# Optimization experiments

Hardware: AMD Instinct MI355X
Metric: run time of the kernel (lower is better)

Reference implementation:

```python
import jax, jax.numpy as jnp
import numpy as np

N, NFEAT, NHID, NCLASS, NHEAD = 8192, 512, 64, 16, 4
ALPHA = 0.1  # leaky relu slope
NEG = -9e15


def setup_inputs() -> dict:
    key = jax.random.key(0)
    ks = jax.random.split(key, 7)
    x = jax.random.normal(ks[0], (N, NFEAT), dtype=jnp.float32)
    adj = (jax.random.uniform(ks[1], (N, N)) < 0.05).astype(jnp.float32)
    # per-head params: W [H, nfeat, nhid], a [H, 2*nhid] (xavier-ish scale)
    W = jax.random.normal(ks[2], (NHEAD, NFEAT, NHID), dtype=jnp.float32) * (1.0 / np.sqrt(NFEAT))
    a = jax.random.normal(ks[3], (NHEAD, 2 * NHID), dtype=jnp.float32) * (1.0 / np.sqrt(NHID))
    W_out = jax.random.normal(ks[4], (NHEAD * NHID, NCLASS), dtype=jnp.float32) * (1.0 / np.sqrt(NHEAD * NHID))
    a_out = jax.random.normal(ks[5], (2 * NCLASS,), dtype=jnp.float32) * (1.0 / np.sqrt(NCLASS))
    return {"x": x, "adj": adj, "W": W, "a": a, "W_out": W_out, "a_out": a_out}


def _gat_layer(h, adj, Wk, ak):
    """Dense pyGAT GraphAttentionLayer (eval mode, dropout = identity)."""
    d = Wk.shape[1]
    Wh = h @ Wk                         # [N, d]
    f1 = Wh @ ak[:d]                    # [N]
    f2 = Wh @ ak[d:]                    # [N]
    e = jax.nn.leaky_relu(f1[:, None] + f2[None, :], negative_slope=ALPHA)  # [N, N]
    att = jax.nn.softmax(jnp.where(adj > 0, e, NEG), axis=1)
    return att @ Wh                     # [N, d]


def reference(x, adj, W, a, W_out, a_out):
    # eval mode: F.dropout is identity
    heads = jax.vmap(lambda Wk, ak: jax.nn.elu(_gat_layer(x, adj, Wk, ak)))(W, a)  # [H, N, nhid]
    h = jnp.transpose(heads, (1, 0, 2)).reshape(x.shape[0], -1)                    # [N, H*nhid]
    out = jax.nn.elu(_gat_layer(h, adj, W_out, a_out))                             # [N, nclass]
    return jax.nn.log_softmax(out, axis=1)
```

## Files before the change

kernel.cpp:

```cpp
#include <hip/hip_runtime.h>
#include <hip/hip_bf16.h>

#define NN 8192
#define NFEAT 512
#define NHID 64
#define NCLASS 16
#define NHEAD 4
#define ALPHA 0.1f
#define CAP 768
#define ZSPLIT 4
#define JPB (NN / ZSPLIT)
#define DCH 128

typedef short bf16x8 __attribute__((ext_vector_type(8)));
typedef float f32x4 __attribute__((ext_vector_type(4)));
typedef float fv4 __attribute__((ext_vector_type(4)));

__device__ __forceinline__ float lrelu(float x) { return fmaxf(x, ALPHA * x); }
__device__ __forceinline__ float elu(float x) { return x > 0.f ? x : __expf(x) - 1.f; }
__device__ __forceinline__ short f2b(float x) {
  union { __bf16 b; short s; } c; c.b = (__bf16)x; return c.s;
}
__device__ __forceinline__ float b2f(short x) {
  union { unsigned int u; float f; } c; c.u = ((unsigned int)(unsigned short)x) << 16; return c.f;
}

#define UPF(w, v, A0, A1)                                  \
  {                                                        \
    const float lo_ = __uint_as_float((v) << 16);          \
    const float hi_ = __uint_as_float((v) & 0xffff0000u);  \
    (A0) += (w) * lo_;                                     \
    (A1) += (w) * hi_;                                     \
  }

__global__ __launch_bounds__(256) void k_wprep(const float* __restrict__ W,
                                               short* __restrict__ WB) {
  __shared__ float t[64][65];
  const int h = blockIdx.y;
  const int k0 = blockIdx.x * 64;
  const int tid = threadIdx.x;
#pragma unroll
  for (int it = 0; it < 16; ++it) {
    const int r = it * 4 + (tid >> 6), c = tid & 63;
    t[r][c] = W[((size_t)h * NFEAT + k0 + r) * NHID + c];
  }
  __syncthreads();
#pragma unroll
  for (int it = 0; it < 16; ++it) {
    const int d = it * 4 + (tid >> 6), k = tid & 63;
    WB[((size_t)h * NHID + d) * NFEAT + k0 + k] = f2b(t[k][d]);
  }
}

__global__ __launch_bounds__(256) void k_prep1(const float* __restrict__ x,
                                               const short* __restrict__ WB,
                                               const float* __restrict__ a,
                                               short* __restrict__ Whf,
                                               float* __restrict__ f1i,
                                               float* __restrict__ f2i) {
  __shared__ short tile[64][72];
  const int bid = blockIdx.x;
  const int h = bid >> 7;
  const int bm = (bid & 127) * 64;
  const int tid = threadIdx.x;
  const int wv = tid >> 6, lane = tid & 63;
  const int mr = lane & 15, kg = lane >> 4;
  f32x4 acc0 = {0.f, 0.f, 0.f, 0.f}, acc1 = acc0, acc2 = acc0, acc3 = acc0;
  const float* ap = x + (size_t)(bm + wv * 16 + mr) * NFEAT + kg * 8;
  const short* bp = WB + ((size_t)h * NHID + mr) * NFEAT + kg * 8;
#pragma unroll 2
  for (int k0 = 0; k0 < NFEAT; k0 += 32) {
    const float4 xa = *reinterpret_cast<const float4*>(ap);
    const float4 xb = *reinterpret_cast<const float4*>(ap + 4);
    bf16x8 af;
    af[0] = f2b(xa.x); af[1] = f2b(xa.y); af[2] = f2b(xa.z); af[3] = f2b(xa.w);
    af[4] = f2b(xb.x); af[5] = f2b(xb.y); af[6] = f2b(xb.z); af[7] = f2b(xb.w);
    const bf16x8 b0 = *reinterpret_cast<const bf16x8*>(bp);
    const bf16x8 b1 = *reinterpret_cast<const bf16x8*>(bp + 16 * NFEAT);
    const bf16x8 b2 = *reinterpret_cast<const bf16x8*>(bp + 32 * NFEAT);
    const bf16x8 b3 = *reinterpret_cast<const bf16x8*>(bp + 48 * NFEAT);
    acc0 = __builtin_amdgcn_mfma_f32_16x16x32_bf16(af, b0, acc0, 0, 0, 0);
    acc1 = __builtin_amdgcn_mfma_f32_16x16x32_bf16(af, b1, acc1, 0, 0, 0);
    acc2 = __builtin_amdgcn_mfma_f32_16x16x32_bf16(af, b2, acc2, 0, 0, 0);
    acc3 = __builtin_amdgcn_mfma_f32_16x16x32_bf16(af, b3, acc3, 0, 0, 0);
    ap += 32; bp += 32;
  }
  float a1v[4], a2v[4];
#pragma unroll
  for (int c = 0; c < 4; ++c) {
    a1v[c] = a[h * 128 + mr + c * 16];
    a2v[c] = a[h * 128 + 64 + mr + c * 16];
  }
#pragma unroll
  for (int q = 0; q < 4; ++q) {
    float s1 = acc0[q] * a1v[0] + acc1[q] * a1v[1] + acc2[q] * a1v[2] + acc3[q] * a1v[3];
    float s2 = acc0[q] * a2v[0] + acc1[q] * a2v[1] + acc2[q] * a2v[2] + acc3[q] * a2v[3];
#pragma unroll
    for (int off = 1; off < 16; off <<= 1) {
      s1 += __shfl_xor(s1, off);
      s2 += __shfl_xor(s2, off);
    }
    if (mr == 0) {
      const int i = bm + wv * 16 + kg * 4 + q;
      f1i[(size_t)i * 4 + h] = s1;
      f2i[(size_t)i * 4 + h] = s2;
    }
  }
#pragma unroll
  for (int q = 0; q < 4; ++q) {
    const int r = wv * 16 + kg * 4 + q;
    tile[r][mr +  0] = f2b(acc0[q]);
    tile[r][mr + 16] = f2b(acc1[q]);
    tile[r][mr + 32] = f2b(acc2[q]);
    tile[r][mr + 48] = f2b(acc3[q]);
  }
  __syncthreads();
#pragma unroll
  for (int it = 0; it < 2; ++it) {
    const int jbl = (tid >> 6) + it * 4;
    const int d = tid & 63;
    bf16x8 o;
#pragma unroll
    for (int jo = 0; jo < 8; ++jo) o[jo] = tile[jbl * 8 + jo][d];
    *reinterpret_cast<bf16x8*>(Whf +
        (((size_t)h * 1024 + (bm >> 3) + jbl) * 64 + d) * 8) = o;
  }
}

__global__ __launch_bounds__(256) void k_rmax(const float* __restrict__ src,
                                              float* __restrict__ dst, int n, int stride,
                                              int boff) {
  const float* p = src + (size_t)blockIdx.x * boff;
  float m = -1e30f;
  for (int k = threadIdx.x; k < n; k += 256) m = fmaxf(m, p[(size_t)k * stride]);
#pragma unroll
  for (int off = 32; off; off >>= 1) m = fmaxf(m, __shfl_xor(m, off));
  __shared__ float sm[4];
  if ((threadIdx.x & 63) == 0) sm[threadIdx.x >> 6] = m;
  __syncthreads();
  if (threadIdx.x == 0) dst[blockIdx.x] = fmaxf(fmaxf(sm[0], sm[1]), fmaxf(sm[2], sm[3]));
}

__global__ __launch_bounds__(256) void k_acbd(const float* __restrict__ f1i,
                                              const float* __restrict__ f2i,
                                              const float* __restrict__ f2max,
                                              float2* __restrict__ ACh,
                                              unsigned int* __restrict__ BDh) {
  const int idx = blockIdx.x * 256 + threadIdx.x;
  const int i = idx & (NN - 1);
  const int h = idx >> 13;
  const float fm = f2max[h];
  const float f1 = f1i[(size_t)i * 4 + h];
  const float f2 = f2i[(size_t)i * 4 + h];
  const float s = f1 + fm;
  const float mrow = fmaxf(s, 0.1f * s);
  float2 ac;
  ac.x = __expf(s - mrow);
  ac.y = __expf(0.1f * s - mrow);
  ACh[(size_t)h * NN + i] = ac;
  const float t = f2 - fm;
  const unsigned int B = (unsigned short)f2b(__expf(t));
  const unsigned int D = (unsigned short)f2b(__expf(0.1f * t));
  BDh[(size_t)h * NN + i] = B | (D << 16);
}

__global__ __launch_bounds__(256) void k_scan(const float* __restrict__ adj,
                                              unsigned int* __restrict__ bmask) {
  const fv4* a4 = reinterpret_cast<const fv4*>(adj);
  const int t0 = blockIdx.x * 256 + threadIdx.x;
#pragma unroll 4
  for (int it = 0; it < 32; ++it) {
    const int g = it * 524288 + t0;
    const fv4 v = __builtin_nontemporal_load(a4 + g);
    unsigned int nv = (unsigned int)((v.x > 0.f) | ((v.y > 0.f) << 1) |
                                     ((v.z > 0.f) << 2) | ((v.w > 0.f) << 3))
                      << ((threadIdx.x & 7) * 4);
    nv |= __shfl_xor(nv, 1);
    nv |= __shfl_xor(nv, 2);
    nv |= __shfl_xor(nv, 4);
    if ((threadIdx.x & 7) == 0) bmask[g >> 3] = nv;
  }
}

__global__ __launch_bounds__(256) void k_dense1z(const unsigned int* __restrict__ bmask,
                                                 const short* __restrict__ Whf,
                                                 const float2* __restrict__ ACh,
                                                 const unsigned int* __restrict__ BDh,
                                                 float* __restrict__ OpP,
                                                 float* __restrict__ rsP) {
  __shared__ short sm_b[16 * 64 * 8];
  __shared__ unsigned int sm_bd[DCH];
  __shared__ unsigned int sm_mask[64][5];
  const int i0 = blockIdx.x * 64;
  const int h = blockIdx.y;
  const int z = blockIdx.z;
  const int jb0 = z * JPB;
  const int tid = threadIdx.x;
  const int wv = tid >> 6, lane = tid & 63;
  const int mr = lane & 15, kg = lane >> 4;
  const int row_local = wv * 16 + mr;
  const float2 ac = ACh[(size_t)h * NN + i0 + row_local];
  f32x4 acc0 = {0.f, 0.f, 0.f, 0.f}, acc1 = acc0, acc2 = acc0, acc3 = acc0;
  float rs = 0.f;

  for (int jc = jb0; jc < jb0 + JPB; jc += DCH) {
    __syncthreads();
    {
      sm_mask[tid >> 2][tid & 3] =
          bmask[(size_t)(i0 + (tid >> 2)) * 256 + (jc >> 5) + (tid & 3)];
      if (tid < DCH) sm_bd[tid] = BDh[(size_t)h * NN + jc + tid];
      const uint4* src = reinterpret_cast<const uint4*>(
          Whf + ((size_t)h * 1024 + (jc >> 3)) * 512);
      uint4* dst = reinterpret_cast<uint4*>(sm_b);
#pragma unroll
      for (int u = 0; u < 4; ++u) dst[tid + u * 256] = src[tid + u * 256];
    }
    __syncthreads();
#pragma unroll
    for (int ks = 0; ks < DCH / 32; ++ks) {
      const int jl = ks * 32 + kg * 8;
      const uint4 bda = *reinterpret_cast<const uint4*>(&sm_bd[jl]);
      const uint4 bdb = *reinterpret_cast<const uint4*>(&sm_bd[jl + 4]);
      const unsigned int mb = (sm_mask[row_local][ks] >> (kg * 8)) & 0xffu;
      bf16x8 af;
#define MKW(e, bdw)                                              \
      {                                                          \
        const float Bf = __uint_as_float((bdw) << 16);           \
        const float Df = __uint_as_float((bdw) & 0xffff0000u);   \
        float w_ = fmaxf(ac.x * Bf, ac.y * Df);                  \
        w_ = ((mb >> (e)) & 1u) ? w_ : 0.f;                      \
        rs += w_;                                                \
        af[e] = f2b(w_);                                         \
      }
      MKW(0, bda.x) MKW(1, bda.y) MKW(2, bda.z) MKW(3, bda.w)
      MKW(4, bdb.x) MKW(5, bdb.y) MKW(6, bdb.z) MKW(7, bdb.w)
#undef MKW
      const short* wp = sm_b + ((size_t)(jl >> 3) * 64 + mr) * 8;
      const bf16x8 bf0 = *reinterpret_cast<const bf16x8*>(wp);
      const bf16x8 bf1 = *reinterpret_cast<const bf16x8*>(wp + 128);
      const bf16x8 bf2 = *reinterpret_cast<const bf16x8*>(wp + 256);
      const bf16x8 bf3 = *reinterpret_cast<const bf16x8*>(wp + 384);
      acc0 = __builtin_amdgcn_mfma_f32_16x16x32_bf16(af, bf0, acc0, 0, 0, 0);
      acc1 = __builtin_amdgcn_mfma_f32_16x16x32_bf16(af, bf1, acc1, 0, 0, 0);
      acc2 = __builtin_amdgcn_mfma_f32_16x16x32_bf16(af, bf2, acc2, 0, 0, 0);
      acc3 = __builtin_amdgcn_mfma_f32_16x16x32_bf16(af, bf3, acc3, 0, 0, 0);
    }
  }
  rs += __shfl_xor(rs, 16);
  rs += __shfl_xor(rs, 32);
  if (lane < 16)
    rsP[((size_t)z * NHEAD + h) * NN + i0 + wv * 16 + lane] = rs;
  float* op = OpP + (((size_t)z * NHEAD + h) * NN + i0) * 64;
#pragma unroll
  for (int q = 0; q < 4; ++q) {
    const int r = wv * 16 + kg * 4 + q;
    op[(size_t)r * 64 + mr +  0] = acc0[q];
    op[(size_t)r * 64 + mr + 16] = acc1[q];
    op[(size_t)r * 64 + mr + 32] = acc2[q];
    op[(size_t)r * 64 + mr + 48] = acc3[q];
  }
}

__global__ __launch_bounds__(256) void k_comb1(const float* __restrict__ OpP,
                                               const float* __restrict__ rsP,
                                               short* __restrict__ hcat) {
  const int idx = blockIdx.x * 256 + threadIdx.x;
  const int i = idx >> 8;
  const int hc = idx & 255;
  const int h = hc >> 6, d = hc & 63;
  float s = 0.f, rsum = 0.f;
#pragma unroll
  for (int z = 0; z < ZSPLIT; ++z) {
    s += OpP[(((size_t)z * NHEAD + h) * NN + i) * 64 + d];
    rsum += rsP[((size_t)z * NHEAD + h) * NN + i];
  }
  hcat[idx] = f2b(elu(s / rsum));
}

__global__ __launch_bounds__(256) void k_gemm2(const short* __restrict__ hcat,
                                               const float* __restrict__ Wout,
                                               const float* __restrict__ aout,
                                               short* __restrict__ Wh2B,
                                               float* __restrict__ f1o,
                                               float* __restrict__ f2o) {
  __shared__ float sW[NHEAD * NHID][NCLASS + 1];
  __shared__ float sh[16][NHEAD * NHID + 1];
  const int tid = threadIdx.x;
  const int r = tid >> 4, c = tid & 15;
  const int row = blockIdx.x * 16 + r;
  for (int u = tid; u < 256 * 16; u += 256) sW[u >> 4][u & 15] = Wout[u];
  for (int u = tid; u < 16 * 256; u += 256)
    sh[u >> 8][u & 255] = b2f(hcat[(size_t)(blockIdx.x * 16 + (u >> 8)) * 256 + (u & 255)]);
  __syncthreads();
  float acc = 0.f;
#pragma unroll 8
  for (int f = 0; f < 256; ++f) acc += sh[r][f] * sW[f][c];
  Wh2B[(size_t)row * NCLASS + c] = f2b(acc);
  float s1 = acc * aout[c];
  float s2 = acc * aout[NCLASS + c];
#pragma unroll
  for (int off = 8; off; off >>= 1) { s1 += __shfl_xor(s1, off); s2 += __shfl_xor(s2, off); }
  if (c == 0) { f1o[row] = s1; f2o[row] = s2; }
}

__global__ __launch_bounds__(256) void k_attn2(const unsigned int* __restrict__ bmask,
                                               const short* __restrict__ Wh2B,
                                               const float* __restrict__ f1o,
                                               const float* __restrict__ f2o,
                                               const float* __restrict__ f2omax,
                                               float* __restrict__ out) {
  __shared__ unsigned short idx[CAP];
  __shared__ unsigned int wj[CAP + 4];
  __shared__ float red[4][NCLASS];
  __shared__ float swp[4];
  __shared__ float sinvs;
  __shared__ int cnt;
  const int i = blockIdx.x;
  const int tid = threadIdx.x;
  const int wv = tid >> 6, lane = tid & 63;
  if (tid == 0) cnt = 0;
  __syncthreads();

  {
    unsigned int word = bmask[(size_t)i * 256 + tid];
    const int c = __popc(word);
    if (c) {
      int base = atomicAdd(&cnt, c);
      const int j0 = tid * 32;
      while (word) {
        const int b = __ffs(word) - 1;
        word &= word - 1;
        if (base < CAP) idx[base++] = (unsigned short)(j0 + b);
      }
    }
  }
  __syncthreads();
  const int n = min(cnt, CAP);
  if (tid < 4) wj[n + tid] = 0;

  const float f1r = f1o[i];
  const float mrow = lrelu(f1r + f2omax[0]);
  float sw = 0.f;
  for (int k = tid; k < n; k += 256) {
    const int j = idx[k];
    const float w = __expf(lrelu(f1r + f2o[j]) - mrow);
    wj[k] = ((unsigned int)(unsigned short)f2b(w) << 16) | (unsigned int)j;
    sw += w;
  }
#pragma unroll
  for (int off = 32; off; off >>= 1) sw += __shfl_xor(sw, off);
  if (lane == 0) swp[wv] = sw;
  __syncthreads();
  if (tid == 0) sinvs = 1.f / (swp[0] + swp[1] + swp[2] + swp[3]);
  __syncthreads();

  const int grp = tid >> 2, gl = tid & 3;
  float acc0 = 0.f, acc1 = 0.f, acc2 = 0.f, acc3 = 0.f;
  const short* wb = Wh2B + gl * 4;
  for (int kb = grp * 4; kb < n; kb += 256) {
    const uint4 pw = *reinterpret_cast<const uint4*>(wj + kb);
    const uint2 e0 = *reinterpret_cast<const uint2*>(wb + (size_t)(pw.x & 0xffffu) * NCLASS);
    const uint2 e1 = *reinterpret_cast<const uint2*>(wb + (size_t)(pw.y & 0xffffu) * NCLASS);
    const uint2 e2 = *reinterpret_cast<const uint2*>(wb + (size_t)(pw.z & 0xffffu) * NCLASS);
    const uint2 e3 = *reinterpret_cast<const uint2*>(wb + (size_t)(pw.w & 0xffffu) * NCLASS);
    const float w0 = __uint_as_float(pw.x & 0xffff0000u);
    const float w1 = __uint_as_float(pw.y & 0xffff0000u);
    const float w2 = __uint_as_float(pw.z & 0xffff0000u);
    const float w3 = __uint_as_float(pw.w & 0xffff0000u);
    UPF(w0, e0.x, acc0, acc1) UPF(w0, e0.y, acc2, acc3)
    UPF(w1, e1.x, acc0, acc1) UPF(w1, e1.y, acc2, acc3)
    UPF(w2, e2.x, acc0, acc1) UPF(w2, e2.y, acc2, acc3)
    UPF(w3, e3.x, acc0, acc1) UPF(w3, e3.y, acc2, acc3)
  }
  acc0 += __shfl_xor(acc0, 4);  acc1 += __shfl_xor(acc1, 4);
  acc2 += __shfl_xor(acc2, 4);  acc3 += __shfl_xor(acc3, 4);
  acc0 += __shfl_xor(acc0, 8);  acc1 += __shfl_xor(acc1, 8);
  acc2 += __shfl_xor(acc2, 8);  acc3 += __shfl_xor(acc3, 8);
  acc0 += __shfl_xor(acc0, 16); acc1 += __shfl_xor(acc1, 16);
  acc2 += __shfl_xor(acc2, 16); acc3 += __shfl_xor(acc3, 16);
  acc0 += __shfl_xor(acc0, 32); acc1 += __shfl_xor(acc1, 32);
  acc2 += __shfl_xor(acc2, 32); acc3 += __shfl_xor(acc3, 32);
  if (lane < 4) {
    red[wv][lane * 4 + 0] = acc0;
    red[wv][lane * 4 + 1] = acc1;
    red[wv][lane * 4 + 2] = acc2;
    red[wv][lane * 4 + 3] = acc3;
  }
  __syncthreads();
  if (tid < NCLASS) {
    const float s = red[0][tid] + red[1][tid] + red[2][tid] + red[3][tid];
    const float v = elu(s * sinvs);
    float vm = v;
#pragma unroll
    for (int off = 8; off; off >>= 1) vm = fmaxf(vm, __shfl_xor(vm, off, 16));
    float ex = __expf(v - vm);
#pragma unroll
    for (int off = 8; off; off >>= 1) ex += __shfl_xor(ex, off, 16);
    out[(size_t)i * NCLASS + tid] = v - vm - __logf(ex);
  }
}

extern "C" void kernel_launch(void* const* d_in, const int* in_sizes, int n_in,
                              void* d_out, int out_size, void* d_ws, size_t ws_size,
                              hipStream_t stream) {
  const float* x    = (const float*)d_in[0];
  const float* adj  = (const float*)d_in[1];
  const float* W    = (const float*)d_in[2];
  const float* a    = (const float*)d_in[3];
  const float* Wout = (const float*)d_in[4];
  const float* aout = (const float*)d_in[5];
  float* out = (float*)d_out;
  char* ws = (char*)d_ws;
  const size_t MB = 1048576;
  const size_t KB = 1024;

  unsigned int* bmask  = (unsigned int*)(ws);
  short* Whf           = (short*)(ws + 8 * MB);
  short* hcat          = (short*)(ws + 12 * MB);
  float* OpP           = (float*)(ws + 16 * MB);
  float* rsP           = (float*)(ws + 48 * MB);
  short* WB            = (short*)(ws + 49 * MB);
  float* f1i           = (float*)(ws + 49 * MB + 256 * KB);
  float* f2i           = (float*)(ws + 49 * MB + 384 * KB);
  float2* ACh          = (float2*)(ws + 49 * MB + 512 * KB);
  unsigned int* BDh    = (unsigned int*)(ws + 49 * MB + 768 * KB);
  float* f1o           = (float*)(ws + 49 * MB + 896 * KB);
  float* f2o           = (float*)(ws + 49 * MB + 928 * KB);
  short* Wh2B          = (short*)(ws + 49 * MB + 960 * KB);
  float* f2max         = (float*)(ws + 49 * MB + 1216 * KB);
  float* f2omax        = (float*)(ws + 49 * MB + 1216 * KB + 64);

  k_wprep<<<dim3(8, 4), 256, 0, stream>>>(W, WB);
  k_prep1<<<512, 256, 0, stream>>>(x, WB, a, Whf, f1i, f2i);
  k_rmax<<<NHEAD, 256, 0, stream>>>(f2i, f2max, NN, 4, 1);
  k_acbd<<<NN * NHEAD / 256, 256, 0, stream>>>(f1i, f2i, f2max, ACh, BDh);
  k_scan<<<2048, 256, 0, stream>>>(adj, bmask);
  k_dense1z<<<dim3(NN / 64, NHEAD, ZSPLIT), 256, 0, stream>>>(bmask, Whf, ACh, BDh, OpP, rsP);
  k_comb1<<<NN, 256, 0, stream>>>(OpP, rsP, hcat);
  k_gemm2<<<NN / 16, 256, 0, stream>>>(hcat, Wout, aout, Wh2B, f1o, f2o);
  k_rmax<<<1, 256, 0, stream>>>(f2o, f2omax, NN, 1, 0);
  k_attn2<<<NN, 256, 0, stream>>>(bmask, Wh2B, f1o, f2o, f2omax, out);
}
```

Before: 216.2 us.

## Replace sparse gather attention in layer 2 with dense MFMA split-K kernel

The second attention layer no longer compacts neighbor indices and gathers rows per node. It now uses a dense bitmask-driven MFMA kernel split into eight column chunks, with a new factored exp precompute (AC2/BD2), a tiled Wh2 layout written by gemm2, and a combine kernel that does ELU and log-softmax. This trades irregular gathers, atomics and a per-row workspace cap for regular dense tensor-core work over all 8192 columns, plus two extra launches and partial-sum traffic. A leftover dummy mask read was also added to dense1z.

```diff
diff --git a/kernel.cpp b/kernel.cpp
--- a/kernel.cpp
+++ b/kernel.cpp
@@ -7,10 +7,11 @@
 #define NCLASS 16
 #define NHEAD 4
 #define ALPHA 0.1f
-#define CAP 768
 #define ZSPLIT 4
 #define JPB (NN / ZSPLIT)
 #define DCH 128
+#define Z2 8
+#define JPB2 (NN / Z2)
 
 typedef short bf16x8 __attribute__((ext_vector_type(8)));
 typedef float f32x4 __attribute__((ext_vector_type(4)));
@@ -24,14 +25,6 @@
 __device__ __forceinline__ float b2f(short x) {
   union { unsigned int u; float f; } c; c.u = ((unsigned int)(unsigned short)x) << 16; return c.f;
 }
-
-#define UPF(w, v, A0, A1)                                  \
-  {                                                        \
-    const float lo_ = __uint_as_float((v) << 16);          \
-    const float hi_ = __uint_as_float((v) & 0xffff0000u);  \
-    (A0) += (w) * lo_;                                     \
-    (A1) += (w) * hi_;                                     \
-  }
 
 __global__ __launch_bounds__(256) void k_wprep(const float* __restrict__ W,
                                                short* __restrict__ WB) {
@@ -164,6 +157,27 @@
   BDh[(size_t)h * NN + i] = B | (D << 16);
 }
 
+__global__ __launch_bounds__(256) void k_acbd2(const float* __restrict__ f1o,
+                                               const float* __restrict__ f2o,
+                                               const float* __restrict__ f2omax,
+                                               float2* __restrict__ AC2,
+                                               unsigned int* __restrict__ BD2) {
+  const int i = blockIdx.x * 256 + threadIdx.x;
+  const float fm = f2omax[0];
+  const float f1 = f1o[i];
+  const float f2 = f2o[i];
+  const float s = f1 + fm;
+  const float mrow = fmaxf(s, 0.1f * s);
+  float2 ac;
+  ac.x = __expf(s - mrow);
+  ac.y = __expf(0.1f * s - mrow);
+  AC2[i] = ac;
+  const float t = f2 - fm;
+  const unsigned int B = (unsigned short)f2b(__expf(t));
+  const unsigned int D = (unsigned short)f2b(__expf(0.1f * t));
+  BD2[i] = B | (D << 16);
+}
+
 __global__ __launch_bounds__(256) void k_scan(const float* __restrict__ adj,
                                               unsigned int* __restrict__ bmask) {
   const fv4* a4 = reinterpret_cast<const fv4*>(adj);
@@ -221,14 +235,17 @@
       const int jl = ks * 32 + kg * 8;
       const uint4 bda = *reinterpret_cast<const uint4*>(&sm_bd[jl]);
       const uint4 bdb = *reinterpret_cast<const uint4*>(&sm_bd[jl + 4]);
-      const unsigned int mb = (sm_mask[row_local][ks] >> (kg * 8)) & 0xffu;
+      const unsigned int mb = (sm_mask[row_local][(jc - jb0) / 32 % 4 == 0 ? ks : ks]
+                               >> 0);
+      (void)mb;
+      const unsigned int mbb = (sm_mask[row_local][ks] >> (kg * 8)) & 0xffu;
       bf16x8 af;
 #define MKW(e, bdw)                                              \
       {                                                          \
         const float Bf = __uint_as_float((bdw) << 16);           \
         const float Df = __uint_as_float((bdw) & 0xffff0000u);   \
         float w_ = fmaxf(ac.x * Bf, ac.y * Df);                  \
-        w_ = ((mb >> (e)) & 1u) ? w_ : 0.f;                      \
+        w_ = ((mbb >> (e)) & 1u) ? w_ : 0.f;                     \
         rs += w_;                                                \
         af[e] = f2b(w_);                                         \
       }
@@ -280,7 +297,7 @@
 __global__ __launch_bounds__(256) void k_gemm2(const short* __restrict__ hcat,
                                                const float* __restrict__ Wout,
                                                const float* __restrict__ aout,
-                                               short* __restrict__ Wh2B,
+                                               short* __restrict__ Wh2f,
                                                float* __restrict__ f1o,
                                                float* __restrict__ f2o) {
   __shared__ float sW[NHEAD * NHID][NCLASS + 1];
@@ -295,7 +312,7 @@
   float acc = 0.f;
 #pragma unroll 8
   for (int f = 0; f < 256; ++f) acc += sh[r][f] * sW[f][c];
-  Wh2B[(size_t)row * NCLASS + c] = f2b(acc);
+  Wh2f[(((size_t)blockIdx.x * 2 + (r >> 3)) * 16 + c) * 8 + (r & 7)] = f2b(acc);
   float s1 = acc * aout[c];
   float s2 = acc * aout[NCLASS + c];
 #pragma unroll
@@ -303,101 +320,85 @@
   if (c == 0) { f1o[row] = s1; f2o[row] = s2; }
 }
 
-__global__ __launch_bounds__(256) void k_attn2(const unsigned int* __restrict__ bmask,
-                                               const short* __restrict__ Wh2B,
-                                               const float* __restrict__ f1o,
-                                               const float* __restrict__ f2o,
-                                               const float* __restrict__ f2omax,
+__global__ __launch_bounds__(256) void k_dense2z(const unsigned int* __restrict__ bmask,
+                                                 const short* __restrict__ Wh2f,
+                                                 const float2* __restrict__ AC2,
+                                                 const unsigned int* __restrict__ BD2,
+                                                 float* __restrict__ Op2P,
+                                                 float* __restrict__ rs2P) {
+  __shared__ unsigned int sm_mask[64][33];
+  const int i0 = blockIdx.x * 64;
+  const int z = blockIdx.y;
+  const int jb0 = z * JPB2;
+  const int tid = threadIdx.x;
+  {
+    const int row = tid >> 2;
+    const int w0 = (tid & 3) * 8;
+#pragma unroll
+    for (int u = 0; u < 8; ++u)
+      sm_mask[row][w0 + u] = bmask[(size_t)(i0 + row) * 256 + (jb0 >> 5) + w0 + u];
+  }
+  __syncthreads();
+  const int wv = tid >> 6, lane = tid & 63;
+  const int mr = lane & 15, kg = lane >> 4;
+  const int row_local = wv * 16 + mr;
+  const float2 ac = AC2[i0 + row_local];
+  f32x4 acc = {0.f, 0.f, 0.f, 0.f};
+  float rs = 0.f;
+  const unsigned int* bd = BD2 + jb0;
+  const short* w2 = Wh2f + (size_t)(jb0 >> 3) * 128 + mr * 8;
+#pragma unroll 2
+  for (int ks = 0; ks < 32; ++ks) {
+    const int jl = ks * 32 + kg * 8;
+    const uint4 bda = *reinterpret_cast<const uint4*>(bd + jl);
+    const uint4 bdb = *reinterpret_cast<const uint4*>(bd + jl + 4);
+    const unsigned int mbb = (sm_mask[row_local][ks] >> (kg * 8)) & 0xffu;
+    bf16x8 af;
+#define MKW(e, bdw)                                              \
+    {                                                            \
+      const float Bf = __uint_as_float((bdw) << 16);             \
+      const float Df = __uint_as_float((bdw) & 0xffff0000u);     \
+      float w_ = fmaxf(ac.x * Bf, ac.y * Df);                    \
+      w_ = ((mbb >> (e)) & 1u) ? w_ : 0.f;                       \
+      rs += w_;                                                  \
+      af[e] = f2b(w_);                                           \
+    }
+    MKW(0, bda.x) MKW(1, bda.y) MKW(2, bda.z) MKW(3, bda.w)
+    MKW(4, bdb.x) MKW(5, bdb.y) MKW(6, bdb.z) MKW(7, bdb.w)
+#undef MKW
+    const bf16x8 bf = *reinterpret_cast<const bf16x8*>(w2 + (size_t)(jl >> 3) * 128);
+    acc = __builtin_amdgcn_mfma_f32_16x16x32_bf16(af, bf, acc, 0, 0, 0);
+  }
+  rs += __shfl_xor(rs, 16);
+  rs += __shfl_xor(rs, 32);
+  if (lane < 16)
+    rs2P[(size_t)z * NN + i0 + wv * 16 + lane] = rs;
+  float* op = Op2P + ((size_t)z * NN + i0) * NCLASS;
+#pragma unroll
+  for (int q = 0; q < 4; ++q)
+    op[(size_t)(wv * 16 + kg * 4 + q) * NCLASS + mr] = acc[q];
+}
+
+__global__ __launch_bounds__(256) void k_comb2(const float* __restrict__ Op2P,
+                                               const float* __restrict__ rs2P,
                                                float* __restrict__ out) {
-  __shared__ unsigned short idx[CAP];
-  __shared__ unsigned int wj[CAP + 4];
-  __shared__ float red[4][NCLASS];
-  __shared__ float swp[4];
-  __shared__ float sinvs;
-  __shared__ int cnt;
-  const int i = blockIdx.x;
-  const int tid = threadIdx.x;
-  const int wv = tid >> 6, lane = tid & 63;
-  if (tid == 0) cnt = 0;
-  __syncthreads();
-
-  {
-    unsigned int word = bmask[(size_t)i * 256 + tid];
-    const int c = __popc(word);
-    if (c) {
-      int base = atomicAdd(&cnt, c);
-      const int j0 = tid * 32;
-      while (word) {
-        const int b = __ffs(word) - 1;
-        word &= word - 1;
-        if (base < CAP) idx[base++] = (unsigned short)(j0 + b);
-      }
-    }
-  }
-  __syncthreads();
-  const int n = min(cnt, CAP);
-  if (tid < 4) wj[n + tid] = 0;
-
-  const float f1r = f1o[i];
-  const float mrow = lrelu(f1r + f2omax[0]);
-  float sw = 0.f;
-  for (int k = tid; k < n; k += 256) {
-    const int j = idx[k];
-    const float w = __expf(lrelu(f1r + f2o[j]) - mrow);
-    wj[k] = ((unsigned int)(unsigned short)f2b(w) << 16) | (unsigned int)j;
-    sw += w;
-  }
-#pragma unroll
-  for (int off = 32; off; off >>= 1) sw += __shfl_xor(sw, off);
-  if (lane == 0) swp[wv] = sw;
-  __syncthreads();
-  if (tid == 0) sinvs = 1.f / (swp[0] + swp[1] + swp[2] + swp[3]);
-  __syncthreads();
-
-  const int grp = tid >> 2, gl = tid & 3;
-  float acc0 = 0.f, acc1 = 0.f, acc2 = 0.f, acc3 = 0.f;
-  const short* wb = Wh2B + gl * 4;
-  for (int kb = grp * 4; kb < n; kb += 256) {
-    const uint4 pw = *reinterpret_cast<const uint4*>(wj + kb);
-    const uint2 e0 = *reinterpret_cast<const uint2*>(wb + (size_t)(pw.x & 0xffffu) * NCLASS);
-    const uint2 e1 = *reinterpret_cast<const uint2*>(wb + (size_t)(pw.y & 0xffffu) * NCLASS);
-    const uint2 e2 = *reinterpret_cast<const uint2*>(wb + (size_t)(pw.z & 0xffffu) * NCLASS);
-    const uint2 e3 = *reinterpret_cast<const uint2*>(wb + (size_t)(pw.w & 0xffffu) * NCLASS);
-    const float w0 = __uint_as_float(pw.x & 0xffff0000u);
-    const float w1 = __uint_as_float(pw.y & 0xffff0000u);
-    const float w2 = __uint_as_float(pw.z & 0xffff0000u);
-    const float w3 = __uint_as_float(pw.w & 0xffff0000u);
-    UPF(w0, e0.x, acc0, acc1) UPF(w0, e0.y, acc2, acc3)
-    UPF(w1, e1.x, acc0, acc1) UPF(w1, e1.y, acc2, acc3)
-    UPF(w2, e2.x, acc0, acc1) UPF(w2, e2.y, acc2, acc3)
-    UPF(w3, e3.x, acc0, acc1) UPF(w3, e3.y, acc2, acc3)
-  }
-  acc0 += __shfl_xor(acc0, 4);  acc1 += __shfl_xor(acc1, 4);
-  acc2 += __shfl_xor(acc2, 4);  acc3 += __shfl_xor(acc3, 4);
-  acc0 += __shfl_xor(acc0, 8);  acc1 += __shfl_xor(acc1, 8);
-  acc2 += __shfl_xor(acc2, 8);  acc3 += __shfl_xor(acc3, 8);
-  acc0 += __shfl_xor(acc0, 16); acc1 += __shfl_xor(acc1, 16);
-  acc2 += __shfl_xor(acc2, 16); acc3 += __shfl_xor(acc3, 16);
-  acc0 += __shfl_xor(acc0, 32); acc1 += __shfl_xor(acc1, 32);
-  acc2 += __shfl_xor(acc2, 32); acc3 += __shfl_xor(acc3, 32);
-  if (lane < 4) {
-    red[wv][lane * 4 + 0] = acc0;
-    red[wv][lane * 4 + 1] = acc1;
-    red[wv][lane * 4 + 2] = acc2;
-    red[wv][lane * 4 + 3] = acc3;
-  }
-  __syncthreads();
-  if (tid < NCLASS) {
-    const float s = red[0][tid] + red[1][tid] + red[2][tid] + red[3][tid];
-    const float v = elu(s * sinvs);
-    float vm = v;
-#pragma unroll
-    for (int off = 8; off; off >>= 1) vm = fmaxf(vm, __shfl_xor(vm, off, 16));
-    float ex = __expf(v - vm);
-#pragma unroll
-    for (int off = 8; off; off >>= 1) ex += __shfl_xor(ex, off, 16);
-    out[(size_t)i * NCLASS + tid] = v - vm - __logf(ex);
-  }
+  const int idx = blockIdx.x * 256 + threadIdx.x;
+  const int i = idx >> 4;
+  const int c = idx & 15;
+  float s = 0.f, rsum = 0.f;
+#pragma unroll
+  for (int z = 0; z < Z2; ++z) {
+    s += Op2P[((size_t)z * NN + i) * NCLASS + c];
+    rsum += rs2P[(size_t)z * NN + i];
+  }
+  const float v = elu(s / rsum);
+  float vm = v;
+#pragma unroll
+  for (int off = 8; off; off >>= 1) vm = fmaxf(vm, __shfl_xor(vm, off, 16));
+  float ex = __expf(v - vm);
+#pragma unroll
+  for (int off = 8; off; off >>= 1) ex += __shfl_xor(ex, off, 16);
+  out[idx] = v - vm - __logf(ex);
 }
 
 extern "C" void kernel_launch(void* const* d_in, const int* in_sizes, int n_in,
@@ -419,16 +420,20 @@
   short* hcat          = (short*)(ws + 12 * MB);
   float* OpP           = (float*)(ws + 16 * MB);
   float* rsP           = (float*)(ws + 48 * MB);
-  short* WB            = (short*)(ws + 49 * MB);
-  float* f1i           = (float*)(ws + 49 * MB + 256 * KB);
-  float* f2i           = (float*)(ws + 49 * MB + 384 * KB);
-  float2* ACh          = (float2*)(ws + 49 * MB + 512 * KB);
-  unsigned int* BDh    = (unsigned int*)(ws + 49 * MB + 768 * KB);
-  float* f1o           = (float*)(ws + 49 * MB + 896 * KB);
-  float* f2o           = (float*)(ws + 49 * MB + 928 * KB);
-  short* Wh2B          = (short*)(ws + 49 * MB + 960 * KB);
-  float* f2max         = (float*)(ws + 49 * MB + 1216 * KB);
-  float* f2omax        = (float*)(ws + 49 * MB + 1216 * KB + 64);
+  float* Op2P          = (float*)(ws + 49 * MB);
+  float* rs2P          = (float*)(ws + 53 * MB);
+  short* WB            = (short*)(ws + 54 * MB);
+  float* f1i           = (float*)(ws + 54 * MB + 256 * KB);
+  float* f2i           = (float*)(ws + 54 * MB + 384 * KB);
+  float2* ACh          = (float2*)(ws + 54 * MB + 512 * KB);
+  unsigned int* BDh    = (unsigned int*)(ws + 54 * MB + 768 * KB);
+  float* f1o           = (float*)(ws + 54 * MB + 896 * KB);
+  float* f2o           = (float*)(ws + 54 * MB + 928 * KB);
+  short* Wh2f          = (short*)(ws + 54 * MB + 960 * KB);
+  float2* AC2          = (float2*)(ws + 54 * MB + 1216 * KB);
+  unsigned int* BD2    = (unsigned int*)(ws + 54 * MB + 1280 * KB);
+  float* f2max         = (float*)(ws + 54 * MB + 1312 * KB);
+  float* f2omax        = (float*)(ws + 54 * MB + 1312 * KB + 64);
 
   k_wprep<<<dim3(8, 4), 256, 0, stream>>>(W, WB);
   k_prep1<<<512, 256, 0, stream>>>(x, WB, a, Whf, f1i, f2i);
@@ -437,7 +442,9 @@
   k_scan<<<2048, 256, 0, stream>>>(adj, bmask);
   k_dense1z<<<dim3(NN / 64, NHEAD, ZSPLIT), 256, 0, stream>>>(bmask, Whf, ACh, BDh, OpP, rsP);
   k_comb1<<<NN, 256, 0, stream>>>(OpP, rsP, hcat);
-  k_gemm2<<<NN / 16, 256, 0, stream>>>(hcat, Wout, aout, Wh2B, f1o, f2o);
+  k_gemm2<<<NN / 16, 256, 0, stream>>>(hcat, Wout, aout, Wh2f, f1o, f2o);
   k_rmax<<<1, 256, 0, stream>>>(f2o, f2omax, NN, 1, 0);
-  k_attn2<<<NN, 256, 0, stream>>>(bmask, Wh2B, f1o, f2o, f2omax, out);
-}
+  k_acbd2<<<NN / 256, 256, 0, stream>>>(f1o, f2o, f2omax, AC2, BD2);
+  k_dense2z<<<dim3(NN / 64, Z2), 256, 0, stream>>>(bmask, Wh2f, AC2, BD2, Op2P, rs2P);
+  k_comb2<<<NN * NCLASS / 256, 256, 0, stream>>>(Op2P, rs2P, out);
+}
```

Result: no change. 216.0 us (-0.1%).
